# Optimization experiments

Hardware: AMD Instinct MI355X
Metric: run time of the kernel (lower is better)

Reference implementation:

```python
import jax, jax.numpy as jnp
import numpy as np

B, F, T, D, S = 8, 256, 512, 40, 4


def setup_inputs() -> dict:
    key = jax.random.key(0)
    k1, k2 = jax.random.split(key)
    embeddings = jax.random.normal(k1, (B, F, T, D), dtype=jnp.float32)
    assignments = jax.random.uniform(k2, (B, F, T, S), dtype=jnp.float32)
    return {"embeddings": embeddings, "assignments": assignments}


def reference(embeddings, assignments):
    b, f, t, d = embeddings.shape
    s = assignments.shape[-1]
    n = f * t
    E = embeddings.reshape(b, n, d)          # (B, N, D)
    V = assignments.reshape(b, n, s)         # (B, N, S)
    # ||VV^T - EE^T||_F^2 summed over batch, via trace identity:
    #   = ||V^T V||_F^2 - 2 ||V^T E||_F^2 + ||E^T E||_F^2
    VtV = jnp.einsum('bns,bnt->bst', V, V)   # (B, S, S)
    VtE = jnp.einsum('bns,bnd->bsd', V, E)   # (B, S, D)
    EtE = jnp.einsum('bnd,bne->bde', E, E)   # (B, D, D)
    fro_sq = jnp.sum(VtV * VtV) - 2.0 * jnp.sum(VtE * VtE) + jnp.sum(EtE * EtE)
    return fro_sq / (b * n)
```

## Files before the change

kernel.cpp:

```cpp
#include <hip/hip_runtime.h>
#include <hip/hip_bf16.h>

#define BATCHES 8
#define NROWS (256 * 512)
#define DE 40
#define SV 4
#define GP 48
#define GSZ (GP * GP)
#define ROWS_PER_BLOCK 1024
#define CHUNKS (NROWS / ROWS_PER_BLOCK)
#define RSTAGE 128
#define NSTAGES (ROWS_PER_BLOCK / RSTAGE)
#define COLBYTES 256
#define TILEBYTES (GP * COLBYTES)
#define NSLOT 352

typedef __attribute__((ext_vector_type(8))) short bf16x8;
typedef __attribute__((ext_vector_type(4))) float f32x4;
typedef __attribute__((ext_vector_type(2))) int i32x2;

__device__ __forceinline__ int pk_bf16(float lo, float hi) {
    __hip_bfloat162 h2 = __float22bfloat162_rn(float2{lo, hi});
    return *reinterpret_cast<int*>(&h2);
}

__global__ __launch_bounds__(256, 4) void gram_kernel(const float* __restrict__ E,
                                                      const float* __restrict__ V,
                                                      float* __restrict__ G) {
    __shared__ __align__(16) char tb[2][TILEBYTES];
    __shared__ float gsum[GSZ];

    const int tid = threadIdx.x;
    const int lane = tid & 63;
    const int wave = tid >> 6;
    const int b = blockIdx.x / CHUNKS;
    const int chunk = blockIdx.x % CHUNKS;
    const size_t row0 = (size_t)chunk * ROWS_PER_BLOCK;

    const float4* __restrict__ Eg = (const float4*)(E + (size_t)b * NROWS * DE) + row0 * 10;
    const float4* __restrict__ Vg = (const float4*)(V + (size_t)b * NROWS * SV) + row0;

    for (int i = tid; i < GSZ; i += 256) gsum[i] = 0.f;
    if (tid < 128) {
        const int bb = tid >> 6, off = (tid & 63) * 16;
        *(float4*)&tb[bb][44 * COLBYTES + off] = make_float4(0.f, 0.f, 0.f, 0.f);
    }

    const int cgA = tid % 11, rgA = tid / 11;
    const int cgB = (tid + 256) % 11, rgB = (tid + 256) / 11;
    const bool hasB = (tid < 96);
    const bool vA = (cgA == 10), vB = (cgB == 10);
    const int pA = vA ? 1 : 10, cA = vA ? 0 : cgA;
    const int pB = vB ? 1 : 10, cB = vB ? 0 : cgB;
    const float4* __restrict__ gA = vA ? Vg : Eg;
    const float4* __restrict__ gB = vB ? Vg : Eg;
    const int oA = 4 * rgA * pA + cA;
    const int oB = 4 * rgB * pB + cB;

    f32x4 acc[6];
    #pragma unroll
    for (int i = 0; i < 6; ++i) acc[i] = (f32x4){0.f, 0.f, 0.f, 0.f};

    float4 a0, a1, a2, a3, b0, b1, b2, b3;
    a0 = gA[oA]; a1 = gA[oA + pA]; a2 = gA[oA + 2 * pA]; a3 = gA[oA + 3 * pA];
    if (hasB) { b0 = gB[oB]; b1 = gB[oB + pB]; b2 = gB[oB + 2 * pB]; b3 = gB[oB + 3 * pB]; }

    const int fcol = lane & 15;
    const int fq = lane >> 4;
    const int foff = ((wave * 64 + fq * 16) + 16 * fcol) & 255;

    int buf = 0;
    for (int s = 0; s < NSTAGES; ++s) {
        __syncthreads();
        {
            char* base = tb[buf];
            #pragma unroll
            for (int j = 0; j < 4; ++j) {
                const float f0 = (j == 0) ? a0.x : (j == 1) ? a0.y : (j == 2) ? a0.z : a0.w;
                const float f1 = (j == 0) ? a1.x : (j == 1) ? a1.y : (j == 2) ? a1.z : a1.w;
                const float f2 = (j == 0) ? a2.x : (j == 1) ? a2.y : (j == 2) ? a2.z : a2.w;
                const float f3 = (j == 0) ? a3.x : (j == 1) ? a3.y : (j == 2) ? a3.z : a3.w;
                const int col = 4 * cgA + j;
                const int off = (8 * rgA + 16 * (col & 15)) & 255;
                i32x2 p = { pk_bf16(f0, f1), pk_bf16(f2, f3) };
                *(i32x2*)&base[col * COLBYTES + off] = p;
            }
            if (hasB) {
                #pragma unroll
                for (int j = 0; j < 4; ++j) {
                    const float f0 = (j == 0) ? b0.x : (j == 1) ? b0.y : (j == 2) ? b0.z : b0.w;
                    const float f1 = (j == 0) ? b1.x : (j == 1) ? b1.y : (j == 2) ? b1.z : b1.w;
                    const float f2 = (j == 0) ? b2.x : (j == 1) ? b2.y : (j == 2) ? b2.z : b2.w;
                    const float f3 = (j == 0) ? b3.x : (j == 1) ? b3.y : (j == 2) ? b3.z : b3.w;
                    const int col = 4 * cgB + j;
                    const int off = (8 * rgB + 16 * (col & 15)) & 255;
                    i32x2 p = { pk_bf16(f0, f1), pk_bf16(f2, f3) };
                    *(i32x2*)&base[col * COLBYTES + off] = p;
                }
            }
        }
        if (s + 1 < NSTAGES) {
            const int adv = (s + 1) * RSTAGE;
            a0 = gA[oA + adv * pA]; a1 = gA[oA + (adv + 1 * 4 / 4) * 0 + oA * 0 + (oA + adv * pA + pA) - (oA + adv * pA)];
            a0 = gA[oA + adv * pA];
            a1 = gA[oA + adv * pA + pA];
            a2 = gA[oA + adv * pA + 2 * pA];
            a3 = gA[oA + adv * pA + 3 * pA];
            if (hasB) {
                b0 = gB[oB + adv * pB];
                b1 = gB[oB + adv * pB + pB];
                b2 = gB[oB + adv * pB + 2 * pB];
                b3 = gB[oB + adv * pB + 3 * pB];
            }
        }
        __syncthreads();

        {
            const char* base = tb[buf];
            const bf16x8 f0 = *(const bf16x8*)&base[(0 * 16 + fcol) * COLBYTES + foff];
            const bf16x8 f1 = *(const bf16x8*)&base[(1 * 16 + fcol) * COLBYTES + foff];
            const bf16x8 f2 = *(const bf16x8*)&base[(2 * 16 + fcol) * COLBYTES + foff];
            acc[0] = __builtin_amdgcn_mfma_f32_16x16x32_bf16(f0, f0, acc[0], 0, 0, 0);
            acc[1] = __builtin_amdgcn_mfma_f32_16x16x32_bf16(f1, f0, acc[1], 0, 0, 0);
            acc[2] = __builtin_amdgcn_mfma_f32_16x16x32_bf16(f1, f1, acc[2], 0, 0, 0);
            acc[3] = __builtin_amdgcn_mfma_f32_16x16x32_bf16(f2, f0, acc[3], 0, 0, 0);
            acc[4] = __builtin_amdgcn_mfma_f32_16x16x32_bf16(f2, f1, acc[4], 0, 0, 0);
            acc[5] = __builtin_amdgcn_mfma_f32_16x16x32_bf16(f2, f2, acc[5], 0, 0, 0);
        }
        buf ^= 1;
    }

    __syncthreads();
    #pragma unroll
    for (int w = 0; w < 4; ++w) {
        if (wave == w) {
            #pragma unroll
            for (int t6 = 0; t6 < 6; ++t6) {
                const int t = (t6 < 1) ? 0 : (t6 < 3) ? 1 : 2;
                const int u = (t6 == 0) ? 0 : (t6 < 3) ? (t6 - 1) : (t6 - 3);
                #pragma unroll
                for (int r = 0; r < 4; ++r) {
                    const int gi = 16 * t + 4 * fq + r;
                    const int gj = 16 * u + fcol;
                    gsum[gi * GP + gj] += acc[t6][r];
                }
            }
        }
        __syncthreads();
    }

    float* Gb = G + (size_t)b * GSZ;
    for (int idx = tid; idx < GSZ; idx += 256) {
        const int gi = idx / GP, gj = idx % GP;
        if (gj <= gi && gi < (DE + SV)) atomicAdd(&Gb[idx], gsum[idx]);
    }
}

__global__ __launch_bounds__(256) void finish_kernel(const float* __restrict__ G,
                                                     float* __restrict__ out) {
    const int tid = threadIdx.x;
    float sum = 0.f;
    for (int idx = tid; idx < BATCHES * GSZ; idx += 256) {
        const int ij = idx % GSZ;
        const int gi = ij / GP;
        const int gj = ij % GP;
        if (gj > gi || gi >= (DE + SV)) continue;
        const float g = G[idx];
        const float w = (gi == gj) ? 1.f : 2.f;
        const float sgn = ((gi < DE) == (gj < DE)) ? 1.f : -1.f;
        sum += w * sgn * g * g;
    }
    #pragma unroll
    for (int o = 32; o > 0; o >>= 1) sum += __shfl_down(sum, o, 64);
    __shared__ float ws[4];
    if ((tid & 63) == 0) ws[tid >> 6] = sum;
    __syncthreads();
    if (tid == 0) {
        const float t = ws[0] + ws[1] + ws[2] + ws[3];
        out[0] = t / (float)((size_t)BATCHES * NROWS);
    }
}

extern "C" void kernel_launch(void* const* d_in, const int* in_sizes, int n_in,
                              void* d_out, int out_size, void* d_ws, size_t ws_size,
                              hipStream_t stream) {
    const float* E = (const float*)d_in[0];
    const float* V = (const float*)d_in[1];
    float* G = (float*)d_ws;

    hipMemsetAsync(G, 0, (size_t)BATCHES * GSZ * sizeof(float), stream);
    gram_kernel<<<BATCHES * CHUNKS, 256, 0, stream>>>(E, V, G);
    finish_kernel<<<1, 256, 0, stream>>>(G, (float*)d_out);
}
```

Before: 269.1 us.

## Restructure staging into single-barrier pipeline and replace atomics with two-pass partial reduction

Measured after the change: 259.4 us. -3.6%, faster.

```diff
diff --git a/kernel.cpp b/kernel.cpp
--- a/kernel.cpp
+++ b/kernel.cpp
@@ -13,7 +13,6 @@
 #define NSTAGES (ROWS_PER_BLOCK / RSTAGE)
 #define COLBYTES 256
 #define TILEBYTES (GP * COLBYTES)
-#define NSLOT 352
 
 typedef __attribute__((ext_vector_type(8))) short bf16x8;
 typedef __attribute__((ext_vector_type(4))) float f32x4;
@@ -26,7 +25,7 @@
 
 __global__ __launch_bounds__(256, 4) void gram_kernel(const float* __restrict__ E,
                                                       const float* __restrict__ V,
-                                                      float* __restrict__ G) {
+                                                      float* __restrict__ P) {
     __shared__ __align__(16) char tb[2][TILEBYTES];
     __shared__ float gsum[GSZ];
 
@@ -61,62 +60,55 @@
     #pragma unroll
     for (int i = 0; i < 6; ++i) acc[i] = (f32x4){0.f, 0.f, 0.f, 0.f};
 
-    float4 a0, a1, a2, a3, b0, b1, b2, b3;
-    a0 = gA[oA]; a1 = gA[oA + pA]; a2 = gA[oA + 2 * pA]; a3 = gA[oA + 3 * pA];
-    if (hasB) { b0 = gB[oB]; b1 = gB[oB + pB]; b2 = gB[oB + 2 * pB]; b3 = gB[oB + 3 * pB]; }
-
     const int fcol = lane & 15;
     const int fq = lane >> 4;
     const int foff = ((wave * 64 + fq * 16) + 16 * fcol) & 255;
 
-    int buf = 0;
+    float4 a0, a1, a2, a3, b0, b1, b2, b3;
+
+#define LOAD_STAGE(sidx)                                                        \
+    {   const int adv = (sidx) * RSTAGE;                                        \
+        a0 = gA[oA + adv * pA];            a1 = gA[oA + adv * pA + pA];         \
+        a2 = gA[oA + adv * pA + 2 * pA];   a3 = gA[oA + adv * pA + 3 * pA];     \
+        if (hasB) {                                                             \
+            b0 = gB[oB + adv * pB];          b1 = gB[oB + adv * pB + pB];       \
+            b2 = gB[oB + adv * pB + 2 * pB]; b3 = gB[oB + adv * pB + 3 * pB];   \
+        } }
+
+#define WRITE_STAGE(bufidx)                                                     \
+    {   char* base = tb[bufidx];                                                \
+        _Pragma("unroll")                                                       \
+        for (int j = 0; j < 4; ++j) {                                           \
+            const float f0 = (j==0)?a0.x:(j==1)?a0.y:(j==2)?a0.z:a0.w;          \
+            const float f1 = (j==0)?a1.x:(j==1)?a1.y:(j==2)?a1.z:a1.w;          \
+            const float f2 = (j==0)?a2.x:(j==1)?a2.y:(j==2)?a2.z:a2.w;          \
+            const float f3 = (j==0)?a3.x:(j==1)?a3.y:(j==2)?a3.z:a3.w;          \
+            const int col = 4 * cgA + j;                                        \
+            const int off = (8 * rgA + 16 * (col & 15)) & 255;                  \
+            i32x2 p = { pk_bf16(f0, f1), pk_bf16(f2, f3) };                     \
+            *(i32x2*)&base[col * COLBYTES + off] = p;                           \
+        }                                                                       \
+        if (hasB) {                                                             \
+            _Pragma("unroll")                                                   \
+            for (int j = 0; j < 4; ++j) {                                       \
+                const float f0 = (j==0)?b0.x:(j==1)?b0.y:(j==2)?b0.z:b0.w;      \
+                const float f1 = (j==0)?b1.x:(j==1)?b1.y:(j==2)?b1.z:b1.w;      \
+                const float f2 = (j==0)?b2.x:(j==1)?b2.y:(j==2)?b2.z:b2.w;      \
+                const float f3 = (j==0)?b3.x:(j==1)?b3.y:(j==2)?b3.z:b3.w;      \
+                const int col = 4 * cgB + j;                                    \
+                const int off = (8 * rgB + 16 * (col & 15)) & 255;              \
+                i32x2 p = { pk_bf16(f0, f1), pk_bf16(f2, f3) };                 \
+                *(i32x2*)&base[col * COLBYTES + off] = p;                       \
+            } } }
+
+    LOAD_STAGE(0);
+    WRITE_STAGE(0);
+    LOAD_STAGE(1);
+    __syncthreads();
+
     for (int s = 0; s < NSTAGES; ++s) {
-        __syncthreads();
         {
-            char* base = tb[buf];
-            #pragma unroll
-            for (int j = 0; j < 4; ++j) {
-                const float f0 = (j == 0) ? a0.x : (j == 1) ? a0.y : (j == 2) ? a0.z : a0.w;
-                const float f1 = (j == 0) ? a1.x : (j == 1) ? a1.y : (j == 2) ? a1.z : a1.w;
-                const float f2 = (j == 0) ? a2.x : (j == 1) ? a2.y : (j == 2) ? a2.z : a2.w;
-                const float f3 = (j == 0) ? a3.x : (j == 1) ? a3.y : (j == 2) ? a3.z : a3.w;
-                const int col = 4 * cgA + j;
-                const int off = (8 * rgA + 16 * (col & 15)) & 255;
-                i32x2 p = { pk_bf16(f0, f1), pk_bf16(f2, f3) };
-                *(i32x2*)&base[col * COLBYTES + off] = p;
-            }
-            if (hasB) {
-                #pragma unroll
-                for (int j = 0; j < 4; ++j) {
-                    const float f0 = (j == 0) ? b0.x : (j == 1) ? b0.y : (j == 2) ? b0.z : b0.w;
-                    const float f1 = (j == 0) ? b1.x : (j == 1) ? b1.y : (j == 2) ? b1.z : b1.w;
-                    const float f2 = (j == 0) ? b2.x : (j == 1) ? b2.y : (j == 2) ? b2.z : b2.w;
-                    const float f3 = (j == 0) ? b3.x : (j == 1) ? b3.y : (j == 2) ? b3.z : b3.w;
-                    const int col = 4 * cgB + j;
-                    const int off = (8 * rgB + 16 * (col & 15)) & 255;
-                    i32x2 p = { pk_bf16(f0, f1), pk_bf16(f2, f3) };
-                    *(i32x2*)&base[col * COLBYTES + off] = p;
-                }
-            }
-        }
-        if (s + 1 < NSTAGES) {
-            const int adv = (s + 1) * RSTAGE;
-            a0 = gA[oA + adv * pA]; a1 = gA[oA + (adv + 1 * 4 / 4) * 0 + oA * 0 + (oA + adv * pA + pA) - (oA + adv * pA)];
-            a0 = gA[oA + adv * pA];
-            a1 = gA[oA + adv * pA + pA];
-            a2 = gA[oA + adv * pA + 2 * pA];
-            a3 = gA[oA + adv * pA + 3 * pA];
-            if (hasB) {
-                b0 = gB[oB + adv * pB];
-                b1 = gB[oB + adv * pB + pB];
-                b2 = gB[oB + adv * pB + 2 * pB];
-                b3 = gB[oB + adv * pB + 3 * pB];
-            }
-        }
-        __syncthreads();
-
-        {
-            const char* base = tb[buf];
+            const char* base = tb[s & 1];
             const bf16x8 f0 = *(const bf16x8*)&base[(0 * 16 + fcol) * COLBYTES + foff];
             const bf16x8 f1 = *(const bf16x8*)&base[(1 * 16 + fcol) * COLBYTES + foff];
             const bf16x8 f2 = *(const bf16x8*)&base[(2 * 16 + fcol) * COLBYTES + foff];
@@ -127,10 +119,11 @@
             acc[4] = __builtin_amdgcn_mfma_f32_16x16x32_bf16(f2, f1, acc[4], 0, 0, 0);
             acc[5] = __builtin_amdgcn_mfma_f32_16x16x32_bf16(f2, f2, acc[5], 0, 0, 0);
         }
-        buf ^= 1;
+        if (s + 1 < NSTAGES) WRITE_STAGE((s + 1) & 1);
+        if (s + 2 < NSTAGES) LOAD_STAGE(s + 2);
+        __syncthreads();
     }
 
-    __syncthreads();
     #pragma unroll
     for (int w = 0; w < 4; ++w) {
         if (wave == w) {
@@ -149,35 +142,37 @@
         __syncthreads();
     }
 
-    float* Gb = G + (size_t)b * GSZ;
-    for (int idx = tid; idx < GSZ; idx += 256) {
-        const int gi = idx / GP, gj = idx % GP;
-        if (gj <= gi && gi < (DE + SV)) atomicAdd(&Gb[idx], gsum[idx]);
-    }
+    const float4* gs4 = (const float4*)gsum;
+    float4* P4 = (float4*)(P + (size_t)blockIdx.x * GSZ);
+    for (int i = tid; i < GSZ / 4; i += 256) P4[i] = gs4[i];
 }
 
-__global__ __launch_bounds__(256) void finish_kernel(const float* __restrict__ G,
+__global__ __launch_bounds__(256) void reduce_finish(const float* __restrict__ P,
                                                      float* __restrict__ out) {
     const int tid = threadIdx.x;
-    float sum = 0.f;
-    for (int idx = tid; idx < BATCHES * GSZ; idx += 256) {
-        const int ij = idx % GSZ;
-        const int gi = ij / GP;
-        const int gj = ij % GP;
-        if (gj > gi || gi >= (DE + SV)) continue;
-        const float g = G[idx];
+    const int b = blockIdx.x / (GSZ / 256);
+    const int e = (blockIdx.x % (GSZ / 256)) * 256 + tid;
+
+    float g = 0.f;
+    const float* base = P + (size_t)b * CHUNKS * GSZ + e;
+    #pragma unroll 4
+    for (int c = 0; c < CHUNKS; ++c) g += base[(size_t)c * GSZ];
+
+    const int gi = e / GP, gj = e % GP;
+    float contrib = 0.f;
+    if (gi < (DE + SV) && gj <= gi) {
         const float w = (gi == gj) ? 1.f : 2.f;
         const float sgn = ((gi < DE) == (gj < DE)) ? 1.f : -1.f;
-        sum += w * sgn * g * g;
+        contrib = w * sgn * g * g;
     }
     #pragma unroll
-    for (int o = 32; o > 0; o >>= 1) sum += __shfl_down(sum, o, 64);
-    __shared__ float ws[4];
-    if ((tid & 63) == 0) ws[tid >> 6] = sum;
+    for (int o = 32; o > 0; o >>= 1) contrib += __shfl_down(contrib, o, 64);
+    __shared__ float ws4[4];
+    if ((tid & 63) == 0) ws4[tid >> 6] = contrib;
     __syncthreads();
     if (tid == 0) {
-        const float t = ws[0] + ws[1] + ws[2] + ws[3];
-        out[0] = t / (float)((size_t)BATCHES * NROWS);
+        const float t = ws4[0] + ws4[1] + ws4[2] + ws4[3];
+        atomicAdd(out, t * (1.f / ((float)BATCHES * (float)NROWS)));
     }
 }
 
@@ -186,9 +181,9 @@
                               hipStream_t stream) {
     const float* E = (const float*)d_in[0];
     const float* V = (const float*)d_in[1];
-    float* G = (float*)d_ws;
+    float* P = (float*)d_ws;
 
-    hipMemsetAsync(G, 0, (size_t)BATCHES * GSZ * sizeof(float), stream);
-    gram_kernel<<<BATCHES * CHUNKS, 256, 0, stream>>>(E, V, G);
-    finish_kernel<<<1, 256, 0, stream>>>(G, (float*)d_out);
+    hipMemsetAsync(d_out, 0, sizeof(float), stream);
+    gram_kernel<<<BATCHES * CHUNKS, 256, 0, stream>>>(E, V, P);
+    reduce_finish<<<BATCHES * (GSZ / 256), 256, 0, stream>>>(P, (float*)d_out);
 }
```
